# Optimization experiments

Hardware: AMD Instinct MI355X
Metric: run time of the kernel (lower is better)

## Reference

```python
import jax, jax.numpy as jnp
import numpy as np

NUM_DEM = 2
VOCAB = 10000
EMB = 128


def setup_inputs() -> dict:
    key = jax.random.key(0)
    k_src, k_emb, k_w1, k_w2 = jax.random.split(key, 4)
    B = 16384
    # 0/1 multi-hot style input (demographic cols also 0/1; math identical)
    src = jax.random.randint(k_src, (B, NUM_DEM + VOCAB), 0, 2).astype(jnp.float32)
    embed = jax.random.normal(k_emb, (VOCAB, EMB), dtype=jnp.float32)
    W1 = jax.random.normal(k_w1, (NUM_DEM + EMB, 16), dtype=jnp.float32) * 0.1
    b1 = jnp.full((16,), 0.01, dtype=jnp.float32)
    W2 = jax.random.normal(k_w2, (16, 2), dtype=jnp.float32) * 0.1
    b2 = jnp.full((2,), 0.01, dtype=jnp.float32)
    return {"src": src, "embed": embed, "W1": W1, "b1": b1, "W2": W2, "b2": b2}


def reference(src, embed, W1, b1, W2, b2):
    dem = src[:, :NUM_DEM]                         # [B, 2]
    codes = src[:, NUM_DEM:].astype(jnp.int32)     # [B, V]
    mask = (codes != 0).astype(embed.dtype)        # multi-hot indicator [B, V]
    counts = jnp.sum(mask, axis=1, keepdims=True)  # [B, 1]
    # fused multi-hot gather + mean pooling (embedding-bag mean)
    pooled = (mask @ embed) / counts               # [B, EMB]
    x = jnp.concatenate([dem, pooled], axis=1)     # [B, 2+EMB]
    h = jnp.tanh(x @ W1 + b1)
    return h @ W2 + b2                             # [B, 2]
```

## Files before the change

### kernel.cpp

```cpp
#include <hip/hip_runtime.h>

#define NUM_DEM 2
#define VOCAB 10000
#define EMB 128
#define NROWS 16384
#define ROWLEN (NUM_DEM + VOCAB)
#define KSTEPS 313
#define PCOLS 132
#define BPACK_USHORTS (KSTEPS * 4096)
#define BPACK_BYTES (BPACK_USHORTS * 2)
#define NCH 6

typedef float f32x4 __attribute__((ext_vector_type(4)));
typedef __bf16 bf16x8 __attribute__((ext_vector_type(8)));
typedef short s16x8 __attribute__((ext_vector_type(8)));

union Frag {
    s16x8 s;
    bf16x8 b;
    unsigned int u[4];
    unsigned short h[8];
};

__device__ __forceinline__ unsigned short f2bf_rtne(float f) {
    unsigned int u = __float_as_uint(f);
    u += 0x7FFFu + ((u >> 16) & 1u);
    return (unsigned short)(u >> 16);
}

__global__ void pack_embed_k(const float* __restrict__ embed,
                             unsigned short* __restrict__ bp) {
    int id = blockIdx.x * blockDim.x + threadIdx.x;
    if (id >= KSTEPS * 8 * 64) return;
    int l = id & 63;
    int c = (id >> 6) & 7;
    int t = id >> 9;
    int kbase = t * 32 + ((l >> 4) * 8);
    int n = c * 16 + (l & 15);
    unsigned short v[8];
#pragma unroll
    for (int j = 0; j < 8; ++j) {
        int k = kbase + j;
        float f = (k < VOCAB) ? embed[(size_t)k * EMB + n] : 0.0f;
        v[j] = f2bf_rtne(f);
    }
    uint4 w;
    w.x = (unsigned int)v[0] | ((unsigned int)v[1] << 16);
    w.y = (unsigned int)v[2] | ((unsigned int)v[3] << 16);
    w.z = (unsigned int)v[4] | ((unsigned int)v[5] << 16);
    w.w = (unsigned int)v[6] | ((unsigned int)v[7] << 16);
    *reinterpret_cast<uint4*>(bp + (size_t)id * 8) = w;
}

typedef const __attribute__((address_space(1))) unsigned int* gas_u32p;
typedef __attribute__((address_space(3))) unsigned int* las_u32p;
#define GLOAD_LDS16(g, l)                                                              \
    __builtin_amdgcn_global_load_lds((gas_u32p)(g), (las_u32p)(l), 16, 0, 0)

#define PERM_A(dst, x0, x1)                                                            \
    dst.u[0] = __builtin_amdgcn_perm(__float_as_uint(x0.y), __float_as_uint(x0.x),     \
                                     0x07060302u);                                     \
    dst.u[1] = __builtin_amdgcn_perm(__float_as_uint(x0.w), __float_as_uint(x0.z),     \
                                     0x07060302u);                                     \
    dst.u[2] = __builtin_amdgcn_perm(__float_as_uint(x1.y), __float_as_uint(x1.x),     \
                                     0x07060302u);                                     \
    dst.u[3] = __builtin_amdgcn_perm(__float_as_uint(x1.w), __float_as_uint(x1.z),     \
                                     0x07060302u);

__global__ __launch_bounds__(256, 6) void main_gemm_k(
    const float* __restrict__ src, const unsigned short* __restrict__ bp,
    float* __restrict__ part, int nch) {
    __shared__ alignas(16) unsigned short ldsB[2 * 4096];

    const int tid = threadIdx.x;
    const int lane = tid & 63;
    const int wid = tid >> 6;
    const int rb = blockIdx.x & 255;
    const int ch = blockIdx.x >> 8;
    const int t0 = (KSTEPS * ch) / nch;
    const int t1 = (KSTEPS * (ch + 1)) / nch;

    const int rowbase = rb * 64 + wid * 16;
    const int arow = rowbase + (lane & 15);
    const int kgrp8 = (lane >> 4) * 8;
    const float* asrc = src + (size_t)arow * ROWLEN + NUM_DEM + kgrp8;

    f32x4 pacc[8];
#pragma unroll
    for (int f = 0; f < 8; ++f) pacc[f] = (f32x4){0.f, 0.f, 0.f, 0.f};
    f32x4 cacc = (f32x4){0.f, 0.f, 0.f, 0.f};

    Frag onesf;
    {
        unsigned short o = ((lane & 15) == 0) ? (unsigned short)0x3F80 : (unsigned short)0;
        unsigned int ow = (unsigned int)o | ((unsigned int)o << 16);
        onesf.u[0] = ow; onesf.u[1] = ow; onesf.u[2] = ow; onesf.u[3] = ow;
    }

    int t = t0;
    for (; t + 2 <= t1; t += 2) {
        const unsigned short* gB0 = bp + (size_t)t * 4096 + wid * 1024 + lane * 8;
        const unsigned short* gB1 = gB0 + 4096;
        unsigned short* lB0 = ldsB + wid * 1024 + lane * 8;
        unsigned short* lB1 = lB0 + 4096;
        GLOAD_LDS16(gB0, lB0);
        GLOAD_LDS16(gB0 + 512, lB0 + 512);
        GLOAD_LDS16(gB1, lB1);
        GLOAD_LDS16(gB1 + 512, lB1 + 512);

        Frag af0, af1;
        {
            f32x4 z = (f32x4){0.f, 0.f, 0.f, 0.f};
            f32x4 a00 = z, a01 = z, a10 = z, a11 = z;
            if (t * 32 + kgrp8 + 8 <= VOCAB) {
                const f32x4* ap = reinterpret_cast<const f32x4*>(asrc + (size_t)t * 32);
                a00 = ap[0];
                a01 = ap[1];
            }
            if ((t + 1) * 32 + kgrp8 + 8 <= VOCAB) {
                const f32x4* ap =
                    reinterpret_cast<const f32x4*>(asrc + (size_t)(t + 1) * 32);
                a10 = ap[0];
                a11 = ap[1];
            }
            PERM_A(af0, a00, a01);
            PERM_A(af1, a10, a11);
        }

        __syncthreads();

#pragma unroll
        for (int f = 0; f < 8; ++f) {
            Frag bfr;
            bfr.s = *reinterpret_cast<const s16x8*>(ldsB + f * 512 + lane * 8);
            pacc[f] = __builtin_amdgcn_mfma_f32_16x16x32_bf16(af0.b, bfr.b, pacc[f], 0, 0, 0);
        }
        cacc = __builtin_amdgcn_mfma_f32_16x16x32_bf16(af0.b, onesf.b, cacc, 0, 0, 0);
#pragma unroll
        for (int f = 0; f < 8; ++f) {
            Frag bfr;
            bfr.s = *reinterpret_cast<const s16x8*>(ldsB + 4096 + f * 512 + lane * 8);
            pacc[f] = __builtin_amdgcn_mfma_f32_16x16x32_bf16(af1.b, bfr.b, pacc[f], 0, 0, 0);
        }
        cacc = __builtin_amdgcn_mfma_f32_16x16x32_bf16(af1.b, onesf.b, cacc, 0, 0, 0);

        __syncthreads();
    }
    if (t < t1) {
        const unsigned short* gB0 = bp + (size_t)t * 4096 + wid * 1024 + lane * 8;
        unsigned short* lB0 = ldsB + wid * 1024 + lane * 8;
        GLOAD_LDS16(gB0, lB0);
        GLOAD_LDS16(gB0 + 512, lB0 + 512);

        Frag af0;
        {
            f32x4 z = (f32x4){0.f, 0.f, 0.f, 0.f};
            f32x4 a00 = z, a01 = z;
            if (t * 32 + kgrp8 + 8 <= VOCAB) {
                const f32x4* ap = reinterpret_cast<const f32x4*>(asrc + (size_t)t * 32);
                a00 = ap[0];
                a01 = ap[1];
            }
            PERM_A(af0, a00, a01);
        }
        __syncthreads();
#pragma unroll
        for (int f = 0; f < 8; ++f) {
            Frag bfr;
            bfr.s = *reinterpret_cast<const s16x8*>(ldsB + f * 512 + lane * 8);
            pacc[f] = __builtin_amdgcn_mfma_f32_16x16x32_bf16(af0.b, bfr.b, pacc[f], 0, 0, 0);
        }
        cacc = __builtin_amdgcn_mfma_f32_16x16x32_bf16(af0.b, onesf.b, cacc, 0, 0, 0);
        __syncthreads();
    }

    const int rlo = (lane >> 4) * 4;
    float* pch = part + (size_t)ch * NROWS * PCOLS;
#pragma unroll
    for (int f = 0; f < 8; ++f) {
#pragma unroll
        for (int r = 0; r < 4; ++r) {
            int row = rowbase + rlo + r;
            pch[(size_t)row * PCOLS + f * 16 + (lane & 15)] = pacc[f][r];
        }
    }
    if ((lane & 15) == 0) {
#pragma unroll
        for (int r = 0; r < 4; ++r) {
            int row = rowbase + rlo + r;
            pch[(size_t)row * PCOLS + 128] = cacc[r];
        }
    }
}

__global__ __launch_bounds__(256) void mlp_k(const float* __restrict__ part,
                                             const float* __restrict__ src,
                                             const float* __restrict__ W1,
                                             const float* __restrict__ b1,
                                             const float* __restrict__ W2,
                                             const float* __restrict__ b2,
                                             float* __restrict__ out, int nch) {
    __shared__ float xls[16][131];
    __shared__ float hls[16][16];
    __shared__ float cnt[16];
    const int tid = threadIdx.x;
    const int rb = blockIdx.x * 16;

    if (tid < 16) {
        float s = 0.f;
        for (int c = 0; c < nch; ++c)
            s += part[((size_t)c * NROWS + rb + tid) * PCOLS + 128];
        cnt[tid] = s;
    }
    if (tid >= 16 && tid < 48) {
        int r = (tid - 16) >> 1, d = (tid - 16) & 1;
        xls[r][d] = src[(size_t)(rb + r) * ROWLEN + d];
    }
    __syncthreads();

    for (int idx = tid; idx < 16 * 128; idx += 256) {
        int r = idx >> 7, col = idx & 127;
        float s = 0.f;
        for (int c = 0; c < nch; ++c)
            s += part[((size_t)c * NROWS + rb + r) * PCOLS + col];
        xls[r][NUM_DEM + col] = s / cnt[r];
    }
    __syncthreads();

    {
        int r = tid >> 4, u = tid & 15;
        float acc = b1[u];
        for (int i = 0; i < NUM_DEM + EMB; ++i) acc += xls[r][i] * W1[i * 16 + u];
        hls[r][u] = tanhf(acc);
    }
    __syncthreads();

    if (tid < 32) {
        int r = tid >> 1, o = tid & 1;
        float acc = b2[o];
#pragma unroll
        for (int u = 0; u < 16; ++u) acc += hls[r][u] * W2[u * 2 + o];
        out[(size_t)(rb + r) * 2 + o] = acc;
    }
}

extern "C" void kernel_launch(void* const* d_in, const int* in_sizes, int n_in,
                              void* d_out, int out_size, void* d_ws, size_t ws_size,
                              hipStream_t stream) {
    const float* src = (const float*)d_in[0];
    const float* embed = (const float*)d_in[1];
    const float* W1 = (const float*)d_in[2];
    const float* b1 = (const float*)d_in[3];
    const float* W2 = (const float*)d_in[4];
    const float* b2 = (const float*)d_in[5];
    float* out = (float*)d_out;

    unsigned short* bpack = (unsigned short*)d_ws;
    float* part = (float*)((char*)d_ws + BPACK_BYTES);

    const size_t part1 = (size_t)NROWS * PCOLS * sizeof(float);
    int nch = NCH;
    while (nch > 1 && BPACK_BYTES + part1 * (size_t)nch > ws_size) nch >>= 1;

    hipLaunchKernelGGL(pack_embed_k, dim3((KSTEPS * 8 * 64 + 255) / 256), dim3(256), 0,
                       stream, embed, bpack);
    hipLaunchKernelGGL(main_gemm_k, dim3(256 * nch), dim3(256), 0, stream, src, bpack,
                       part, nch);
    hipLaunchKernelGGL(mlp_k, dim3(NROWS / 16), dim3(256), 0, stream, part, src, W1, b1,
                       W2, b2, out, nch);
}
```

Before: 215.6 us.

## Switch main GEMM to 32x32x16 MFMA with 128-row blocks and scalar counts

The embedding-bag GEMM moves from 16x16x32 to 32x32x16 bf16 MFMA tiles, with each wave covering 32 rows and blocks covering 128 rows. The packed embedding layout is changed to match the new B fragment order. Row counts are now summed directly from the fp32 A values instead of through an extra ones-vector MFMA. K-chunks rise from 6 to 8 and the occupancy hint drops to 4, trading more register pressure and a larger partial buffer for fewer LDS reads of B per FLOP and less MFMA overhead.

```diff
diff --git a/kernel.cpp b/kernel.cpp
--- a/kernel.cpp
+++ b/kernel.cpp
@@ -8,10 +8,11 @@
 #define KSTEPS 313
 #define PCOLS 132
 #define BPACK_USHORTS (KSTEPS * 4096)
-#define BPACK_BYTES (BPACK_USHORTS * 2)
-#define NCH 6
+#define BPACK_BYTES ((size_t)BPACK_USHORTS * 2)
+#define NCH 8
 
 typedef float f32x4 __attribute__((ext_vector_type(4)));
+typedef float f32x16 __attribute__((ext_vector_type(16)));
 typedef __bf16 bf16x8 __attribute__((ext_vector_type(8)));
 typedef short s16x8 __attribute__((ext_vector_type(8)));
 
@@ -19,7 +20,6 @@
     s16x8 s;
     bf16x8 b;
     unsigned int u[4];
-    unsigned short h[8];
 };
 
 __device__ __forceinline__ unsigned short f2bf_rtne(float f) {
@@ -33,10 +33,11 @@
     int id = blockIdx.x * blockDim.x + threadIdx.x;
     if (id >= KSTEPS * 8 * 64) return;
     int l = id & 63;
-    int c = (id >> 6) & 7;
+    int kf = (id >> 6) & 1;
+    int cf = (id >> 7) & 3;
     int t = id >> 9;
-    int kbase = t * 32 + ((l >> 4) * 8);
-    int n = c * 16 + (l & 15);
+    int kbase = t * 32 + kf * 16 + ((l >> 5) * 8);
+    int n = cf * 32 + (l & 31);
     unsigned short v[8];
 #pragma unroll
     for (int j = 0; j < 8; ++j) {
@@ -67,7 +68,20 @@
     dst.u[3] = __builtin_amdgcn_perm(__float_as_uint(x1.w), __float_as_uint(x1.z),     \
                                      0x07060302u);
 
-__global__ __launch_bounds__(256, 6) void main_gemm_k(
+#define LOAD_A(dst, T_, KF)                                                            \
+    {                                                                                  \
+        f32x4 x0 = (f32x4){0.f, 0.f, 0.f, 0.f}, x1 = x0;                               \
+        int base_ = (T_)*32 + (KF)*16;                                                 \
+        if (base_ + klo + 8 <= VOCAB) {                                                \
+            const f32x4* ap_ = reinterpret_cast<const f32x4*>(asrc + base_);           \
+            x0 = ap_[0];                                                               \
+            x1 = ap_[1];                                                               \
+        }                                                                              \
+        cnt += x0.x + x0.y + x0.z + x0.w + x1.x + x1.y + x1.z + x1.w;                  \
+        PERM_A(dst, x0, x1);                                                           \
+    }
+
+__global__ __launch_bounds__(256, 4) void main_gemm_k(
     const float* __restrict__ src, const unsigned short* __restrict__ bp,
     float* __restrict__ part, int nch) {
     __shared__ alignas(16) unsigned short ldsB[2 * 4096];
@@ -75,27 +89,22 @@
     const int tid = threadIdx.x;
     const int lane = tid & 63;
     const int wid = tid >> 6;
-    const int rb = blockIdx.x & 255;
-    const int ch = blockIdx.x >> 8;
+    const int rb = blockIdx.x & 127;
+    const int ch = blockIdx.x >> 7;
     const int t0 = (KSTEPS * ch) / nch;
     const int t1 = (KSTEPS * (ch + 1)) / nch;
 
-    const int rowbase = rb * 64 + wid * 16;
-    const int arow = rowbase + (lane & 15);
-    const int kgrp8 = (lane >> 4) * 8;
-    const float* asrc = src + (size_t)arow * ROWLEN + NUM_DEM + kgrp8;
-
-    f32x4 pacc[8];
-#pragma unroll
-    for (int f = 0; f < 8; ++f) pacc[f] = (f32x4){0.f, 0.f, 0.f, 0.f};
-    f32x4 cacc = (f32x4){0.f, 0.f, 0.f, 0.f};
-
-    Frag onesf;
-    {
-        unsigned short o = ((lane & 15) == 0) ? (unsigned short)0x3F80 : (unsigned short)0;
-        unsigned int ow = (unsigned int)o | ((unsigned int)o << 16);
-        onesf.u[0] = ow; onesf.u[1] = ow; onesf.u[2] = ow; onesf.u[3] = ow;
-    }
+    const int rowbase = rb * 128 + wid * 32;
+    const int arow = rowbase + (lane & 31);
+    const int klo = (lane >> 5) * 8;
+    const float* asrc = src + (size_t)arow * ROWLEN + NUM_DEM + klo;
+
+    f32x16 pacc[4];
+#pragma unroll
+    for (int cf = 0; cf < 4; ++cf)
+#pragma unroll
+        for (int r = 0; r < 16; ++r) pacc[cf][r] = 0.f;
+    float cnt = 0.f;
 
     int t = t0;
     for (; t + 2 <= t1; t += 2) {
@@ -108,41 +117,29 @@
         GLOAD_LDS16(gB1, lB1);
         GLOAD_LDS16(gB1 + 512, lB1 + 512);
 
-        Frag af0, af1;
-        {
-            f32x4 z = (f32x4){0.f, 0.f, 0.f, 0.f};
-            f32x4 a00 = z, a01 = z, a10 = z, a11 = z;
-            if (t * 32 + kgrp8 + 8 <= VOCAB) {
-                const f32x4* ap = reinterpret_cast<const f32x4*>(asrc + (size_t)t * 32);
-                a00 = ap[0];
-                a01 = ap[1];
+        Frag af[2][2];
+        LOAD_A(af[0][0], t, 0);
+        LOAD_A(af[0][1], t, 1);
+        LOAD_A(af[1][0], t + 1, 0);
+        LOAD_A(af[1][1], t + 1, 1);
+
+        __syncthreads();
+
+#pragma unroll
+        for (int s = 0; s < 2; ++s) {
+#pragma unroll
+            for (int cf = 0; cf < 4; ++cf) {
+#pragma unroll
+                for (int kf = 0; kf < 2; ++kf) {
+                    Frag bfr;
+                    bfr.s = *reinterpret_cast<const s16x8*>(ldsB + s * 4096 +
+                                                            (cf * 2 + kf) * 512 +
+                                                            lane * 8);
+                    pacc[cf] = __builtin_amdgcn_mfma_f32_32x32x16_bf16(
+                        af[s][kf].b, bfr.b, pacc[cf], 0, 0, 0);
+                }
             }
-            if ((t + 1) * 32 + kgrp8 + 8 <= VOCAB) {
-                const f32x4* ap =
-                    reinterpret_cast<const f32x4*>(asrc + (size_t)(t + 1) * 32);
-                a10 = ap[0];
-                a11 = ap[1];
-            }
-            PERM_A(af0, a00, a01);
-            PERM_A(af1, a10, a11);
         }
-
-        __syncthreads();
-
-#pragma unroll
-        for (int f = 0; f < 8; ++f) {
-            Frag bfr;
-            bfr.s = *reinterpret_cast<const s16x8*>(ldsB + f * 512 + lane * 8);
-            pacc[f] = __builtin_amdgcn_mfma_f32_16x16x32_bf16(af0.b, bfr.b, pacc[f], 0, 0, 0);
-        }
-        cacc = __builtin_amdgcn_mfma_f32_16x16x32_bf16(af0.b, onesf.b, cacc, 0, 0, 0);
-#pragma unroll
-        for (int f = 0; f < 8; ++f) {
-            Frag bfr;
-            bfr.s = *reinterpret_cast<const s16x8*>(ldsB + 4096 + f * 512 + lane * 8);
-            pacc[f] = __builtin_amdgcn_mfma_f32_16x16x32_bf16(af1.b, bfr.b, pacc[f], 0, 0, 0);
-        }
-        cacc = __builtin_amdgcn_mfma_f32_16x16x32_bf16(af1.b, onesf.b, cacc, 0, 0, 0);
 
         __syncthreads();
     }
@@ -152,45 +149,37 @@
         GLOAD_LDS16(gB0, lB0);
         GLOAD_LDS16(gB0 + 512, lB0 + 512);
 
-        Frag af0;
-        {
-            f32x4 z = (f32x4){0.f, 0.f, 0.f, 0.f};
-            f32x4 a00 = z, a01 = z;
-            if (t * 32 + kgrp8 + 8 <= VOCAB) {
-                const f32x4* ap = reinterpret_cast<const f32x4*>(asrc + (size_t)t * 32);
-                a00 = ap[0];
-                a01 = ap[1];
+        Frag af[2];
+        LOAD_A(af[0], t, 0);
+        LOAD_A(af[1], t, 1);
+        __syncthreads();
+#pragma unroll
+        for (int cf = 0; cf < 4; ++cf) {
+#pragma unroll
+            for (int kf = 0; kf < 2; ++kf) {
+                Frag bfr;
+                bfr.s = *reinterpret_cast<const s16x8*>(ldsB + (cf * 2 + kf) * 512 +
+                                                        lane * 8);
+                pacc[cf] = __builtin_amdgcn_mfma_f32_32x32x16_bf16(af[kf].b, bfr.b,
+                                                                   pacc[cf], 0, 0, 0);
             }
-            PERM_A(af0, a00, a01);
         }
         __syncthreads();
-#pragma unroll
-        for (int f = 0; f < 8; ++f) {
-            Frag bfr;
-            bfr.s = *reinterpret_cast<const s16x8*>(ldsB + f * 512 + lane * 8);
-            pacc[f] = __builtin_amdgcn_mfma_f32_16x16x32_bf16(af0.b, bfr.b, pacc[f], 0, 0, 0);
+    }
+
+    const int rlo = 4 * (lane >> 5);
+    const int col = lane & 31;
+    float* pch = part + (size_t)ch * NROWS * PCOLS;
+#pragma unroll
+    for (int cf = 0; cf < 4; ++cf) {
+#pragma unroll
+        for (int r = 0; r < 16; ++r) {
+            int row = rowbase + (r & 3) + 8 * (r >> 2) + rlo;
+            pch[(size_t)row * PCOLS + cf * 32 + col] = pacc[cf][r];
         }
-        cacc = __builtin_amdgcn_mfma_f32_16x16x32_bf16(af0.b, onesf.b, cacc, 0, 0, 0);
-        __syncthreads();
-    }
-
-    const int rlo = (lane >> 4) * 4;
-    float* pch = part + (size_t)ch * NROWS * PCOLS;
-#pragma unroll
-    for (int f = 0; f < 8; ++f) {
-#pragma unroll
-        for (int r = 0; r < 4; ++r) {
-            int row = rowbase + rlo + r;
-            pch[(size_t)row * PCOLS + f * 16 + (lane & 15)] = pacc[f][r];
-        }
-    }
-    if ((lane & 15) == 0) {
-#pragma unroll
-        for (int r = 0; r < 4; ++r) {
-            int row = rowbase + rlo + r;
-            pch[(size_t)row * PCOLS + 128] = cacc[r];
-        }
-    }
+    }
+    float tot = cnt + __shfl_xor(cnt, 32);
+    if (lane < 32) pch[(size_t)(rowbase + lane) * PCOLS + 128] = tot;
 }
 
 __global__ __launch_bounds__(256) void mlp_k(const float* __restrict__ part,
@@ -264,7 +253,7 @@
 
     hipLaunchKernelGGL(pack_embed_k, dim3((KSTEPS * 8 * 64 + 255) / 256), dim3(256), 0,
                        stream, embed, bpack);
-    hipLaunchKernelGGL(main_gemm_k, dim3(256 * nch), dim3(256), 0, stream, src, bpack,
+    hipLaunchKernelGGL(main_gemm_k, dim3(128 * nch), dim3(256), 0, stream, src, bpack,
                        part, nch);
     hipLaunchKernelGGL(mlp_k, dim3(NROWS / 16), dim3(256), 0, stream, part, src, W1, b1,
                        W2, b2, out, nch);
```

New measurement: 250.4 us. 16.1% more time.
